# Kernel optimization log

Hardware: AMD Instinct MI355X
Metric: run time of the kernel (lower is better)

## Reference

```python
import jax, jax.numpy as jnp
import numpy as np

N_NODES = 200000
H_DIM = 64
OUT_DIM = 32
NUM_RELS = 8
NUM_BASES = 8
N_EDGES = 1000000


def setup_inputs() -> dict:
    key = jax.random.key(0)
    ks = jax.random.split(key, 10)
    emb = jax.random.normal(ks[0], (N_NODES, H_DIM), dtype=jnp.float32) * 0.1
    basis1 = jax.random.normal(ks[1], (NUM_BASES, H_DIM, H_DIM), dtype=jnp.float32) * 0.05
    comp1 = jax.random.normal(ks[2], (NUM_RELS, NUM_BASES), dtype=jnp.float32)
    bias1 = jnp.zeros((H_DIM,), dtype=jnp.float32)
    basis2 = jax.random.normal(ks[3], (NUM_BASES, H_DIM, OUT_DIM), dtype=jnp.float32) * 0.05
    comp2 = jax.random.normal(ks[4], (NUM_RELS, NUM_BASES), dtype=jnp.float32)
    bias2 = jnp.zeros((OUT_DIM,), dtype=jnp.float32)
    src = jax.random.randint(ks[5], (N_EDGES,), 0, N_NODES, dtype=jnp.int32)
    dst = jax.random.randint(ks[6], (N_EDGES,), 0, N_NODES, dtype=jnp.int32)
    etype = jax.random.randint(ks[7], (N_EDGES,), 0, NUM_RELS, dtype=jnp.int32)
    norm = jax.random.uniform(ks[8], (N_EDGES, 1), dtype=jnp.float32)
    return {"emb": emb, "basis1": basis1, "comp1": comp1, "bias1": bias1,
            "basis2": basis2, "comp2": comp2, "bias2": bias2,
            "src": src, "dst": dst, "etype": etype, "norm": norm}


def _rel_graph_conv(x, basis, comp, bias, src, dst, etype, norm, num_nodes):
    # basis regularizer: W_r = sum_b comp[r,b] * basis[b]  -> [R, in, out]
    W = jnp.einsum('rb,bio->rio', comp, basis)
    # transform all nodes under every relation: [R, N, out]
    y = jnp.einsum('ni,rio->rno', x, W)
    # per-edge message: gather transformed src feature for the edge's relation
    msg = y[etype, src] * norm  # [E, out]
    # scatter-sum to destination nodes
    agg = jax.ops.segment_sum(msg, dst, num_segments=num_nodes)
    return agg + bias


def reference(emb, basis1, comp1, bias1, basis2, comp2, bias2, src, dst, etype, norm):
    h = _rel_graph_conv(emb, basis1, comp1, bias1, src, dst, etype, norm, emb.shape[0])
    h = _rel_graph_conv(h, basis2, comp2, bias2, src, dst, etype, norm, emb.shape[0])
    return h
```

## Files before the change

kernel.cpp:

```cpp
#include <hip/hip_runtime.h>
#include <hip/hip_bf16.h>

#define NRELS 8
#define NB 8
#define PBLK 256
#define BSH 9
#define BCAP 3584

typedef __attribute__((ext_vector_type(8))) short short8v;
typedef __attribute__((ext_vector_type(4))) float f32x4;

__device__ __forceinline__ short bfc(float f) {
    __hip_bfloat16 h = __float2bfloat16(f);
    return *reinterpret_cast<short*>(&h);
}
__device__ __forceinline__ float bf2f(ushort u) {
    return __uint_as_float((unsigned)u << 16);
}
__device__ __forceinline__ short8v cvt8(float4 a, float4 b) {
    short8v r;
    r[0] = bfc(a.x); r[1] = bfc(a.y); r[2] = bfc(a.z); r[3] = bfc(a.w);
    r[4] = bfc(b.x); r[5] = bfc(b.y); r[6] = bfc(b.z); r[7] = bfc(b.w);
    return r;
}

__global__ void wprep_kernel(const float* __restrict__ basis1, const float* __restrict__ comp1,
                             const float* __restrict__ basis2, const float* __restrict__ comp2,
                             short* __restrict__ Wf1, short* __restrict__ Wf2) {
    int idx = blockIdx.x * blockDim.x + threadIdx.x;
    const int n1 = 64 * 512;
    const int n2 = 32 * 512;
    if (idx < n1) {
        int f = idx >> 9, lane = (idx >> 3) & 63, j = idx & 7;
        int ks = f & 1, q = (f >> 1) & 7, gg = f >> 4;
        int c = gg * 128 + 8 * (lane & 15) + q;
        int k = ks * 32 + (lane >> 4) * 8 + j;
        int r = c >> 6, crel = c & 63;
        float s = 0.f;
#pragma unroll
        for (int b = 0; b < NB; ++b)
            s = fmaf(comp1[r * NB + b], basis1[b * 4096 + k * 64 + crel], s);
        Wf1[idx] = bfc(s);
    } else if (idx < n1 + n2) {
        int i2 = idx - n1;
        int f = i2 >> 9, lane = (i2 >> 3) & 63, j = i2 & 7;
        int ks = f & 1, q = (f >> 1) & 7, gg = f >> 4;
        int c = gg * 128 + 8 * (lane & 15) + q;
        int k = ks * 32 + (lane >> 4) * 8 + j;
        int r = c >> 5, crel = c & 31;
        float s = 0.f;
#pragma unroll
        for (int b = 0; b < NB; ++b)
            s = fmaf(comp2[r * NB + b], basis2[b * 2048 + k * 32 + crel], s);
        Wf2[i2] = bfc(s);
    }
}

__global__ void histA_kernel(const int* __restrict__ dst, int* __restrict__ histM,
                             int nEdges, int nBuck, int chunk) {
    __shared__ int h[512];
    for (int t = threadIdx.x; t < nBuck; t += 256) h[t] = 0;
    __syncthreads();
    int start = blockIdx.x * chunk;
    int end = min(nEdges, start + chunk);
    for (int i = start + threadIdx.x; i < end; i += 256)
        atomicAdd(&h[dst[i] >> BSH], 1);
    __syncthreads();
    for (int t = threadIdx.x; t < nBuck; t += 256)
        histM[t * PBLK + blockIdx.x] = h[t];
}

__global__ void scanA_kernel(const int* __restrict__ histM, int* __restrict__ offs,
                             int* __restrict__ bucketBase, int nBuck, int nBlk, int nEdges) {
    __shared__ int tot[512];
    const int b = threadIdx.x;
    int s = 0;
    if (b < nBuck) {
        const int4* hp = (const int4*)(histM + b * nBlk);
        for (int k = 0; k < nBlk / 4; ++k) {
            int4 v = hp[k];
            s += v.x + v.y + v.z + v.w;
        }
    }
    tot[b] = s;
    __syncthreads();
    int own = s;
    for (int st = 1; st < 512; st <<= 1) {
        int t = (b >= st) ? tot[b - st] : 0;
        __syncthreads();
        tot[b] += t;
        __syncthreads();
    }
    int base = tot[b] - own;
    if (b < nBuck) {
        bucketBase[b] = base;
        int run = base;
        const int4* hp = (const int4*)(histM + b * nBlk);
        int4* op = (int4*)(offs + b * nBlk);
        for (int k = 0; k < nBlk / 4; ++k) {
            int4 h4 = hp[k];
            int4 o4;
            o4.x = run; run += h4.x;
            o4.y = run; run += h4.y;
            o4.z = run; run += h4.z;
            o4.w = run; run += h4.w;
            op[k] = o4;
        }
    }
    if (b == 0) bucketBase[nBuck] = nEdges;
}

__global__ void part_kernel(const int* __restrict__ src, const int* __restrict__ dst,
                            const int* __restrict__ et, const float* __restrict__ norm,
                            const int* __restrict__ offs, uint2* __restrict__ staged,
                            int nEdges, int nBuck, int chunk) {
    __shared__ int cur[512];
    for (int t = threadIdx.x; t < nBuck; t += 256)
        cur[t] = offs[t * PBLK + blockIdx.x];
    __syncthreads();
    int start = blockIdx.x * chunk;
    int end = min(nEdges, start + chunk);
    for (int i = start + threadIdx.x; i < end; i += 256) {
        int d = dst[i];
        int b = d >> BSH;
        int p = atomicAdd(&cur[b], 1);
        staged[p] = make_uint2(((unsigned)(d & 511) << 21) |
                               ((unsigned)src[i] << 3) | (unsigned)et[i],
                               __float_as_uint(norm[i]));
    }
}

__global__ void sortB_kernel(uint2* __restrict__ meta, const int* __restrict__ bucketBase,
                             int* __restrict__ endOff, int nNodes) {
    const int b = blockIdx.x;
    const int tid = threadIdx.x;
    const int e0 = bucketBase[b];
    const int n = min(bucketBase[b + 1] - e0, BCAP);
    __shared__ uint2 st[BCAP];
    __shared__ int h[512];
    __shared__ int pb[256];
    h[2 * tid] = 0; h[2 * tid + 1] = 0;
    __syncthreads();
    for (int j = tid; j < n; j += 256) {
        uint2 v = meta[e0 + j];
        st[j] = v;
        atomicAdd(&h[v.x >> 21], 1);
    }
    __syncthreads();
    int h0 = h[2 * tid], h1v = h[2 * tid + 1];
    int ps = h0 + h1v;
    pb[tid] = ps;
    __syncthreads();
    for (int s = 1; s < 256; s <<= 1) {
        int t = (tid >= s) ? pb[tid - s] : 0;
        __syncthreads();
        pb[tid] += t;
        __syncthreads();
    }
    int ex = pb[tid] - ps;
    int d0 = b << BSH;
    int dA = d0 + 2 * tid, dB = dA + 1;
    if (dA < nNodes) endOff[dA] = e0 + ex + h0;
    if (dB < nNodes) endOff[dB] = e0 + ex + ps;
    h[2 * tid] = ex;
    h[2 * tid + 1] = ex + h0;
    __syncthreads();
    for (int j = tid; j < n; j += 256) {
        uint2 v = st[j];
        int r = atomicAdd(&h[v.x >> 21], 1);
        meta[e0 + r] = make_uint2(v.x & 0x1FFFFFu, v.y);
    }
}

template <int G128, bool BF16IN>
__global__ __launch_bounds__(256) void transform_kernel(
    const void* __restrict__ xin, const short* __restrict__ Wf,
    ushort* __restrict__ yb, int nNodes) {
    constexpr int TOUT = G128 * 128;
    const int lane = threadIdx.x & 63;
    const int wid = (blockIdx.x * blockDim.x + threadIdx.x) >> 6;
    const int base = wid * 32;
    if (base >= nNodes) return;
    const int ml = lane & 15, kg = lane >> 4;

    short8v A[2][2];
#pragma unroll
    for (int s = 0; s < 2; ++s) {
        int row = min(base + s * 16 + ml, nNodes - 1);
        if (BF16IN) {
            const ushort* xp = (const ushort*)xin + (size_t)row * 64 + kg * 8;
            A[s][0] = *(const short8v*)xp;
            A[s][1] = *(const short8v*)(xp + 32);
        } else {
            const float* xp = (const float*)xin + (size_t)row * 64 + kg * 8;
            float4 f0 = *(const float4*)xp;
            float4 f1 = *(const float4*)(xp + 4);
            float4 f2 = *(const float4*)(xp + 32);
            float4 f3 = *(const float4*)(xp + 36);
            A[s][0] = cvt8(f0, f1);
            A[s][1] = cvt8(f2, f3);
        }
    }
#pragma unroll
    for (int gg = 0; gg < G128; ++gg) {
        const short* wp = Wf + (size_t)gg * 16 * 512 + lane * 8;
        f32x4 acc[2][8];
#pragma unroll
        for (int q = 0; q < 8; ++q) {
            short8v B0 = *(const short8v*)(wp + (q * 2 + 0) * 512);
            short8v B1 = *(const short8v*)(wp + (q * 2 + 1) * 512);
#pragma unroll
            for (int s = 0; s < 2; ++s) {
                acc[s][q] = __builtin_amdgcn_mfma_f32_16x16x32_bf16(A[s][0], B0,
                                                                    (f32x4){0.f, 0.f, 0.f, 0.f}, 0, 0, 0);
                acc[s][q] = __builtin_amdgcn_mfma_f32_16x16x32_bf16(A[s][1], B1, acc[s][q], 0, 0, 0);
            }
        }
#pragma unroll
        for (int s = 0; s < 2; ++s) {
#pragma unroll
            for (int i = 0; i < 4; ++i) {
                int row = base + s * 16 + kg * 4 + i;
                if (row < nNodes) {
                    uint4 pk;
                    pk.x = (unsigned)(ushort)bfc(acc[s][0][i]) | ((unsigned)(ushort)bfc(acc[s][1][i]) << 16);
                    pk.y = (unsigned)(ushort)bfc(acc[s][2][i]) | ((unsigned)(ushort)bfc(acc[s][3][i]) << 16);
                    pk.z = (unsigned)(ushort)bfc(acc[s][4][i]) | ((unsigned)(ushort)bfc(acc[s][5][i]) << 16);
                    pk.w = (unsigned)(ushort)bfc(acc[s][6][i]) | ((unsigned)(ushort)bfc(acc[s][7][i]) << 16);
                    *reinterpret_cast<uint4*>(yb + (size_t)row * TOUT + gg * 128 + ml * 8) = pk;
                }
            }
        }
    }
}

template <int OUT, typename OutT, bool ACCUM, bool FILTER, int SHIFT>
__global__ __launch_bounds__(256, 4) void edge_kernel(
    const ushort* __restrict__ yb, const uint2* __restrict__ meta,
    const int* __restrict__ endOff, const float* __restrict__ bias,
    OutT* __restrict__ out, int nNodes, int D, int rtLo) {
    const int lane = threadIdx.x & 63;

    if constexpr (!FILTER) {
        const int wid = (blockIdx.x * blockDim.x + threadIdx.x) >> 6;
        const int o = lane & (OUT - 1);
        const int d0 = wid * D;
        if (d0 >= nNodes) return;
        const int d1 = min(d0 + D, nNodes);
        const float bv = bias[o];

        int bndv = 0x7fffffff;
        if (lane < D) bndv = endOff[min(d0 + lane, nNodes - 1)];
        const int eEnd = __builtin_amdgcn_readlane(bndv, d1 - 1 - d0);
        int e = __builtin_amdgcn_readfirstlane((d0 == 0) ? 0 : endOff[d0 - 1]);
        int dcur = d0;
        int bnd = __builtin_amdgcn_readlane(bndv, 0);
        float acc = 0.f;

        auto gv = [&](unsigned key) -> float {
            const ushort* rowp = (const ushort*)((const char*)yb +
                                                 ((size_t)key << SHIFT));
            return bf2f(rowp[o]);
        };
        auto flushd = [&]() {
            size_t idx = (size_t)dcur * OUT + o;
            if (OUT == 64 || lane < OUT) {
                if constexpr (ACCUM)
                    out[idx] = (OutT)(ushort)bfc(bf2f((ushort)out[idx]) + acc);
                else if constexpr (sizeof(OutT) == 2)
                    out[idx] = (OutT)(ushort)bfc(bv + acc);
                else
                    out[idx] = (OutT)(bv + acc);
            }
            acc = 0.f;
            ++dcur;
            bnd = __builtin_amdgcn_readlane(bndv, dcur - d0);
        };

        if (e < eEnd) {
            const int eL = eEnd - 1;
            uint2 Ma[8], Mb[8];
            float Va[8];
#pragma unroll
            for (int k = 0; k < 8; ++k) Ma[k] = meta[min(e + k, eL)];
#pragma unroll
            for (int k = 0; k < 8; ++k) Mb[k] = meta[min(e + 8 + k, eL)];
#pragma unroll
            for (int k = 0; k < 8; ++k) Va[k] = gv(Ma[k].x);

            const int nFull = (eEnd - e) >> 3;
            for (int blk = 0; blk < nFull; ++blk) {
                float Vb[8];
                uint2 Mc[8];
#pragma unroll
                for (int k = 0; k < 8; ++k) Vb[k] = gv(Mb[k].x);
#pragma unroll
                for (int k = 0; k < 8; ++k) Mc[k] = meta[min(e + 16 + k, eL)];
#pragma unroll
                for (int k = 0; k < 8; ++k) {
                    while (e >= bnd) flushd();
                    acc = fmaf(__uint_as_float(Ma[k].y), Va[k], acc);
                    ++e;
                }
#pragma unroll
                for (int k = 0; k < 8; ++k) { Ma[k] = Mb[k]; Mb[k] = Mc[k]; Va[k] = Vb[k]; }
            }
            const int rem = eEnd - e;
#pragma unroll
            for (int k = 0; k < 8; ++k) {
                if (k < rem) {
                    while (e >= bnd) flushd();
                    acc = fmaf(__uint_as_float(Ma[k].y), Va[k], acc);
                    ++e;
                }
            }
        }
        while (dcur < d1) flushd();
    } else {
        constexpr int GPW = 64 / OUT;
        const int wid = (blockIdx.x * blockDim.x + threadIdx.x) >> 6;
        const int sub = (GPW == 2) ? (lane >> 5) : 0;
        const int gbase = sub << 5;
        const int gid = wid * GPW + sub;
        const int o = lane & (OUT - 1);
        const int d0 = gid * D;
        if (d0 >= nNodes) return;
        const int d1 = min(d0 + D, nNodes);
        const float bv = bias[o];

        int bndv = 0x7fffffff;
        if (o < D) bndv = endOff[min(d0 + o, nNodes - 1)];
        const int eEnd = __shfl(bndv, gbase + (d1 - 1 - d0));
        int e = (d0 == 0) ? 0 : endOff[d0 - 1];
        int dcur = d0;
        int bnd = __shfl(bndv, gbase);
        float acc = 0.f;

        auto gv = [&](unsigned key) -> float {
            int rr = (int)(key & 7u) - rtLo;
            if ((unsigned)rr >= 4u) return 0.f;
            unsigned off = (((key >> 3) * (unsigned)(4 * OUT)) +
                            (unsigned)rr * OUT + (unsigned)o) << 1;
            return bf2f(*(const ushort*)((const char*)yb + off));
        };
        auto flush = [&](int d, float a) {
            size_t idx = (size_t)d * OUT + o;
            if constexpr (ACCUM) {
                out[idx] = (OutT)(ushort)bfc(bf2f((ushort)out[idx]) + a);
            } else if constexpr (sizeof(OutT) == 2) {
                out[idx] = (OutT)(ushort)bfc(bv + a);
            } else {
                out[idx] = (OutT)(bv + a);
            }
        };

        if (e < eEnd) {
            const int eL = eEnd - 1;
            uint2 Ma[8], Mb[8];
            float Va[8];
#pragma unroll
            for (int k = 0; k < 8; ++k) Ma[k] = meta[min(e + k, eL)];
#pragma unroll
            for (int k = 0; k < 8; ++k) Mb[k] = meta[min(e + 8 + k, eL)];
#pragma unroll
            for (int k = 0; k < 8; ++k) Va[k] = gv(Ma[k].x);
            const int nFull = (eEnd - e) >> 3;
            for (int blk = 0; blk < nFull; ++blk) {
                float Vb[8];
                uint2 Mc[8];
#pragma unroll
                for (int k = 0; k < 8; ++k) Vb[k] = gv(Mb[k].x);
#pragma unroll
                for (int k = 0; k < 8; ++k) Mc[k] = meta[min(e + 16 + k, eL)];
#pragma unroll
                for (int k = 0; k < 8; ++k) {
                    while (e >= bnd) {
                        flush(dcur, acc); acc = 0.f; ++dcur;
                        bnd = __shfl(bndv, gbase + (dcur - d0));
                    }
                    acc = fmaf(__uint_as_float(Ma[k].y), Va[k], acc);
                    ++e;
                }
#pragma unroll
                for (int k = 0; k < 8; ++k) { Ma[k] = Mb[k]; Mb[k] = Mc[k]; Va[k] = Vb[k]; }
            }
            const int rem = eEnd - e;
#pragma unroll
            for (int k = 0; k < 8; ++k) {
                if (k < rem) {
                    while (e >= bnd) {
                        flush(dcur, acc); acc = 0.f; ++dcur;
                        bnd = __shfl(bndv, gbase + (dcur - d0));
                    }
                    acc = fmaf(__uint_as_float(Ma[k].y), Va[k], acc);
                    ++e;
                }
            }
        }
        for (; dcur < d1; ++dcur) {
            flush(dcur, acc);
            acc = 0.f;
        }
    }
}

extern "C" void kernel_launch(void* const* d_in, const int* in_sizes, int n_in,
                              void* d_out, int out_size, void* d_ws, size_t ws_size,
                              hipStream_t stream) {
    const float* emb    = (const float*)d_in[0];
    const float* basis1 = (const float*)d_in[1];
    const float* comp1  = (const float*)d_in[2];
    const float* bias1  = (const float*)d_in[3];
    const float* basis2 = (const float*)d_in[4];
    const float* comp2  = (const float*)d_in[5];
    const float* bias2  = (const float*)d_in[6];
    const int*   src    = (const int*)d_in[7];
    const int*   dst    = (const int*)d_in[8];
    const int*   etype  = (const int*)d_in[9];
    const float* norm   = (const float*)d_in[10];
    float* out = (float*)d_out;

    const int nNodes = in_sizes[0] / 64;
    const int nEdges = in_sizes[7];

    const int nBuck = (nNodes + 511) >> BSH;
    const int chunk = (nEdges + PBLK - 1) / PBLK;

    char* ws = (char*)d_ws;
    short* Wf1        = (short*)(ws);
    short* Wf2        = (short*)(ws + 65536);
    int*   histM      = (int*)(ws + 98304);
    int*   offs       = (int*)(ws + 498688);
    int*   bucketBase = (int*)(ws + 899072);
    int*   endOff     = (int*)(ws + 900640);
    size_t offMeta = 1703936;
    uint2* meta       = (uint2*)(ws + offMeta);
    size_t offY = offMeta + (size_t)nEdges * 8;

    const size_t yFused = (size_t)nNodes * 512 * 2;
    const size_t yHalf  = (size_t)nNodes * 256 * 2;
    const size_t h1Sz   = (size_t)nNodes * 64 * 2;
    const bool fused = ws_size >= offY + yFused + h1Sz;
    const size_t ySz = fused ? yFused : yHalf;
    ushort* yB  = (ushort*)(ws + offY);
    ushort* h1b = (ushort*)(ws + offY + ySz);

    wprep_kernel<<<192, 256, 0, stream>>>(basis1, comp1, basis2, comp2, Wf1, Wf2);
    histA_kernel<<<PBLK, 256, 0, stream>>>(dst, histM, nEdges, nBuck, chunk);
    scanA_kernel<<<1, 512, 0, stream>>>(histM, offs, bucketBase, nBuck, PBLK, nEdges);
    part_kernel<<<PBLK, 256, 0, stream>>>(src, dst, etype, norm, offs, meta,
                                          nEdges, nBuck, chunk);
    sortB_kernel<<<nBuck, 256, 0, stream>>>(meta, bucketBase, endOff, nNodes);

    const int tBlocks = (((nNodes + 31) / 32) + 3) / 4;
    const int D = 8;
    const int nGroups = (nNodes + D - 1) / D;
    const int gBlocks = (nGroups + 3) / 4;

    if (fused) {
        transform_kernel<4, false><<<tBlocks, 256, 0, stream>>>(emb, Wf1, yB, nNodes);
        edge_kernel<64, ushort, false, false, 7><<<gBlocks, 256, 0, stream>>>(
            yB, meta, endOff, bias1, h1b, nNodes, D, 0);
    } else {
        transform_kernel<2, false><<<tBlocks, 256, 0, stream>>>(emb, Wf1, yB, nNodes);
        edge_kernel<64, ushort, false, true, 0><<<gBlocks, 256, 0, stream>>>(
            yB, meta, endOff, bias1, h1b, nNodes, D, 0);
        transform_kernel<2, false><<<tBlocks, 256, 0, stream>>>(emb, Wf1 + 16384, yB, nNodes);
        edge_kernel<64, ushort, true, true, 0><<<gBlocks, 256, 0, stream>>>(
            yB, meta, endOff, bias1, h1b, nNodes, D, 4);
    }
    transform_kernel<2, true><<<tBlocks, 256, 0, stream>>>(h1b, Wf2, yB, nNodes);
    edge_kernel<32, float, false, false, 6><<<gBlocks, 256, 0, stream>>>(
        yB, meta, endOff, bias2, out, nNodes, D, 0);
}
```

Measured before the change: 244.1 us.

## Co-schedule layer-1 transform with sort preprocessing and split layer-2 pipeline

Splits the layer-1 node transform into four slices and fuses each slice into the histogram, scan, partition and bucket-sort launches as extra blocks. The small sort kernels then share the GPU with independent dense work instead of leaving CUs idle. It also splits layer-1 aggregation into node halves, so the layer-2 transform of the first half runs alongside the edge aggregation of the second half. This needs an extra y2 buffer and uses hand-tuned split ratios.

```diff
diff --git a/kernel.cpp b/kernel.cpp
--- a/kernel.cpp
+++ b/kernel.cpp
@@ -56,69 +56,81 @@
     }
 }
 
-__global__ void histA_kernel(const int* __restrict__ dst, int* __restrict__ histM,
-                             int nEdges, int nBuck, int chunk) {
+__device__ __forceinline__ void histA_body(const int* __restrict__ dst, int* __restrict__ histM,
+                                           int nEdges, int nBuck, int chunk, int bid) {
     __shared__ int h[512];
     for (int t = threadIdx.x; t < nBuck; t += 256) h[t] = 0;
     __syncthreads();
-    int start = blockIdx.x * chunk;
+    int start = bid * chunk;
     int end = min(nEdges, start + chunk);
     for (int i = start + threadIdx.x; i < end; i += 256)
         atomicAdd(&h[dst[i] >> BSH], 1);
     __syncthreads();
     for (int t = threadIdx.x; t < nBuck; t += 256)
-        histM[t * PBLK + blockIdx.x] = h[t];
-}
-
-__global__ void scanA_kernel(const int* __restrict__ histM, int* __restrict__ offs,
-                             int* __restrict__ bucketBase, int nBuck, int nBlk, int nEdges) {
+        histM[t * PBLK + bid] = h[t];
+}
+
+__device__ __forceinline__ void scanA_body(const int* __restrict__ histM, int* __restrict__ offs,
+                                           int* __restrict__ bucketBase, int nBuck, int nBlk,
+                                           int nEdges) {
     __shared__ int tot[512];
-    const int b = threadIdx.x;
-    int s = 0;
-    if (b < nBuck) {
-        const int4* hp = (const int4*)(histM + b * nBlk);
-        for (int k = 0; k < nBlk / 4; ++k) {
-            int4 v = hp[k];
-            s += v.x + v.y + v.z + v.w;
-        }
-    }
-    tot[b] = s;
-    __syncthreads();
-    int own = s;
+    const int tid = threadIdx.x;
+    int sums[2] = {0, 0};
+#pragma unroll
+    for (int half = 0; half < 2; ++half) {
+        int b = tid + half * 256;
+        if (b < nBuck) {
+            const int4* hp = (const int4*)(histM + b * nBlk);
+            int s = 0;
+            for (int k = 0; k < nBlk / 4; ++k) {
+                int4 v = hp[k];
+                s += v.x + v.y + v.z + v.w;
+            }
+            sums[half] = s;
+        }
+        tot[b] = sums[half];
+    }
+    __syncthreads();
     for (int st = 1; st < 512; st <<= 1) {
-        int t = (b >= st) ? tot[b - st] : 0;
+        int t0 = (tid >= st) ? tot[tid - st] : 0;
+        int t1 = tot[tid + 256 - st];
         __syncthreads();
-        tot[b] += t;
+        tot[tid] += t0;
+        tot[tid + 256] += t1;
         __syncthreads();
     }
-    int base = tot[b] - own;
-    if (b < nBuck) {
-        bucketBase[b] = base;
-        int run = base;
-        const int4* hp = (const int4*)(histM + b * nBlk);
-        int4* op = (int4*)(offs + b * nBlk);
-        for (int k = 0; k < nBlk / 4; ++k) {
-            int4 h4 = hp[k];
-            int4 o4;
-            o4.x = run; run += h4.x;
-            o4.y = run; run += h4.y;
-            o4.z = run; run += h4.z;
-            o4.w = run; run += h4.w;
-            op[k] = o4;
-        }
-    }
-    if (b == 0) bucketBase[nBuck] = nEdges;
-}
-
-__global__ void part_kernel(const int* __restrict__ src, const int* __restrict__ dst,
-                            const int* __restrict__ et, const float* __restrict__ norm,
-                            const int* __restrict__ offs, uint2* __restrict__ staged,
-                            int nEdges, int nBuck, int chunk) {
+#pragma unroll
+    for (int half = 0; half < 2; ++half) {
+        int b = tid + half * 256;
+        if (b < nBuck) {
+            int base = tot[b] - sums[half];
+            bucketBase[b] = base;
+            int run = base;
+            const int4* hp = (const int4*)(histM + b * nBlk);
+            int4* op = (int4*)(offs + b * nBlk);
+            for (int k = 0; k < nBlk / 4; ++k) {
+                int4 h4 = hp[k];
+                int4 o4;
+                o4.x = run; run += h4.x;
+                o4.y = run; run += h4.y;
+                o4.z = run; run += h4.z;
+                o4.w = run; run += h4.w;
+                op[k] = o4;
+            }
+        }
+    }
+    if (tid == 0) bucketBase[nBuck] = nEdges;
+}
+
+__device__ __forceinline__ void part_body(const int* __restrict__ src, const int* __restrict__ dst,
+                                          const int* __restrict__ et, const float* __restrict__ norm,
+                                          const int* __restrict__ offs, uint2* __restrict__ staged,
+                                          int nEdges, int nBuck, int chunk, int bid) {
     __shared__ int cur[512];
     for (int t = threadIdx.x; t < nBuck; t += 256)
-        cur[t] = offs[t * PBLK + blockIdx.x];
-    __syncthreads();
-    int start = blockIdx.x * chunk;
+        cur[t] = offs[t * PBLK + bid];
+    __syncthreads();
+    int start = bid * chunk;
     int end = min(nEdges, start + chunk);
     for (int i = start + threadIdx.x; i < end; i += 256) {
         int d = dst[i];
@@ -130,12 +142,12 @@
     }
 }
 
-__global__ void sortB_kernel(uint2* __restrict__ meta, const int* __restrict__ bucketBase,
-                             int* __restrict__ endOff, int nNodes) {
-    const int b = blockIdx.x;
+__device__ __forceinline__ void sortB_body(uint2* __restrict__ meta,
+                                           const int* __restrict__ bucketBase,
+                                           int* __restrict__ endOff, int nNodes, int bid) {
     const int tid = threadIdx.x;
-    const int e0 = bucketBase[b];
-    const int n = min(bucketBase[b + 1] - e0, BCAP);
+    const int e0 = bucketBase[bid];
+    const int n = min(bucketBase[bid + 1] - e0, BCAP);
     __shared__ uint2 st[BCAP];
     __shared__ int h[512];
     __shared__ int pb[256];
@@ -158,7 +170,7 @@
         __syncthreads();
     }
     int ex = pb[tid] - ps;
-    int d0 = b << BSH;
+    int d0 = bid << BSH;
     int dA = d0 + 2 * tid, dB = dA + 1;
     if (dA < nNodes) endOff[dA] = e0 + ex + h0;
     if (dB < nNodes) endOff[dB] = e0 + ex + ps;
@@ -173,12 +185,11 @@
 }
 
 template <int G128, bool BF16IN>
-__global__ __launch_bounds__(256) void transform_kernel(
-    const void* __restrict__ xin, const short* __restrict__ Wf,
-    ushort* __restrict__ yb, int nNodes) {
+__device__ __forceinline__ void transform_body(const void* __restrict__ xin,
+                                               const short* __restrict__ Wf,
+                                               ushort* __restrict__ yb, int nNodes, int wid) {
     constexpr int TOUT = G128 * 128;
     const int lane = threadIdx.x & 63;
-    const int wid = (blockIdx.x * blockDim.x + threadIdx.x) >> 6;
     const int base = wid * 32;
     if (base >= nNodes) return;
     const int ml = lane & 15, kg = lane >> 4;
@@ -234,174 +245,206 @@
     }
 }
 
-template <int OUT, typename OutT, bool ACCUM, bool FILTER, int SHIFT>
-__global__ __launch_bounds__(256, 4) void edge_kernel(
+template <int G128, bool BF16IN>
+__global__ __launch_bounds__(256) void transform_kernel(
+    const void* __restrict__ xin, const short* __restrict__ Wf,
+    ushort* __restrict__ yb, int nNodes, int waveOff) {
+    int wid = waveOff + blockIdx.x * 4 + (threadIdx.x >> 6);
+    transform_body<G128, BF16IN>(xin, Wf, yb, nNodes, wid);
+}
+
+template <int OUT, typename OutT, bool ACCUM, int SHIFT>
+__device__ __forceinline__ void edge_body(const ushort* __restrict__ yb,
+                                          const uint2* __restrict__ meta,
+                                          const int* __restrict__ endOff,
+                                          const float* __restrict__ bias,
+                                          OutT* __restrict__ out, int nNodes, int D,
+                                          int wid, int dLo, int dHi) {
+    const int lane = threadIdx.x & 63;
+    const int o = lane & (OUT - 1);
+    const int d0 = dLo + wid * D;
+    if (d0 >= dHi) return;
+    const int d1 = min(d0 + D, dHi);
+    const float bv = bias[o];
+
+    int bndv = 0x7fffffff;
+    if (lane < D) bndv = endOff[min(d0 + lane, nNodes - 1)];
+    const int eEnd = __builtin_amdgcn_readlane(bndv, d1 - 1 - d0);
+    int e = __builtin_amdgcn_readfirstlane((d0 == 0) ? 0 : endOff[d0 - 1]);
+    int dcur = d0;
+    int bnd = __builtin_amdgcn_readlane(bndv, 0);
+    float acc = 0.f;
+
+    auto gv = [&](unsigned key) -> float {
+        const ushort* rowp = (const ushort*)((const char*)yb + ((size_t)key << SHIFT));
+        return bf2f(rowp[o]);
+    };
+    auto flushd = [&]() {
+        size_t idx = (size_t)dcur * OUT + o;
+        if (OUT == 64 || lane < OUT) {
+            if constexpr (ACCUM)
+                out[idx] = (OutT)(ushort)bfc(bf2f((ushort)out[idx]) + acc);
+            else if constexpr (sizeof(OutT) == 2)
+                out[idx] = (OutT)(ushort)bfc(bv + acc);
+            else
+                out[idx] = (OutT)(bv + acc);
+        }
+        acc = 0.f;
+        ++dcur;
+        bnd = __builtin_amdgcn_readlane(bndv, dcur - d0);
+    };
+
+    if (e < eEnd) {
+        const int eL = eEnd - 1;
+        uint2 Ma[8], Mb[8];
+        float Va[8];
+#pragma unroll
+        for (int k = 0; k < 8; ++k) Ma[k] = meta[min(e + k, eL)];
+#pragma unroll
+        for (int k = 0; k < 8; ++k) Mb[k] = meta[min(e + 8 + k, eL)];
+#pragma unroll
+        for (int k = 0; k < 8; ++k) Va[k] = gv(Ma[k].x);
+
+        const int nFull = (eEnd - e) >> 3;
+        for (int blk = 0; blk < nFull; ++blk) {
+            float Vb[8];
+            uint2 Mc[8];
+#pragma unroll
+            for (int k = 0; k < 8; ++k) Vb[k] = gv(Mb[k].x);
+#pragma unroll
+            for (int k = 0; k < 8; ++k) Mc[k] = meta[min(e + 16 + k, eL)];
+#pragma unroll
+            for (int k = 0; k < 8; ++k) {
+                while (e >= bnd) flushd();
+                acc = fmaf(__uint_as_float(Ma[k].y), Va[k], acc);
+                ++e;
+            }
+#pragma unroll
+            for (int k = 0; k < 8; ++k) { Ma[k] = Mb[k]; Mb[k] = Mc[k]; Va[k] = Vb[k]; }
+        }
+        const int rem = eEnd - e;
+#pragma unroll
+        for (int k = 0; k < 8; ++k) {
+            if (k < rem) {
+                while (e >= bnd) flushd();
+                acc = fmaf(__uint_as_float(Ma[k].y), Va[k], acc);
+                ++e;
+            }
+        }
+    }
+    while (dcur < d1) flushd();
+}
+
+template <int OUT, typename OutT, int SHIFT>
+__global__ __launch_bounds__(256, 4) void edge_s_kernel(
+    const ushort* __restrict__ yb, const uint2* __restrict__ meta,
+    const int* __restrict__ endOff, const float* __restrict__ bias,
+    OutT* __restrict__ out, int nNodes, int dLo, int dHi) {
+    int wid = blockIdx.x * 4 + (threadIdx.x >> 6);
+    edge_body<OUT, OutT, false, SHIFT>(yb, meta, endOff, bias, out, nNodes, 8, wid, dLo, dHi);
+}
+
+template <int OUT, typename OutT, bool ACCUM>
+__global__ __launch_bounds__(256, 4) void edge_f_kernel(
     const ushort* __restrict__ yb, const uint2* __restrict__ meta,
     const int* __restrict__ endOff, const float* __restrict__ bias,
     OutT* __restrict__ out, int nNodes, int D, int rtLo) {
     const int lane = threadIdx.x & 63;
-
-    if constexpr (!FILTER) {
-        const int wid = (blockIdx.x * blockDim.x + threadIdx.x) >> 6;
-        const int o = lane & (OUT - 1);
-        const int d0 = wid * D;
-        if (d0 >= nNodes) return;
-        const int d1 = min(d0 + D, nNodes);
-        const float bv = bias[o];
-
-        int bndv = 0x7fffffff;
-        if (lane < D) bndv = endOff[min(d0 + lane, nNodes - 1)];
-        const int eEnd = __builtin_amdgcn_readlane(bndv, d1 - 1 - d0);
-        int e = __builtin_amdgcn_readfirstlane((d0 == 0) ? 0 : endOff[d0 - 1]);
-        int dcur = d0;
-        int bnd = __builtin_amdgcn_readlane(bndv, 0);
-        float acc = 0.f;
-
-        auto gv = [&](unsigned key) -> float {
-            const ushort* rowp = (const ushort*)((const char*)yb +
-                                                 ((size_t)key << SHIFT));
-            return bf2f(rowp[o]);
-        };
-        auto flushd = [&]() {
-            size_t idx = (size_t)dcur * OUT + o;
-            if (OUT == 64 || lane < OUT) {
-                if constexpr (ACCUM)
-                    out[idx] = (OutT)(ushort)bfc(bf2f((ushort)out[idx]) + acc);
-                else if constexpr (sizeof(OutT) == 2)
-                    out[idx] = (OutT)(ushort)bfc(bv + acc);
-                else
-                    out[idx] = (OutT)(bv + acc);
-            }
-            acc = 0.f;
-            ++dcur;
-            bnd = __builtin_amdgcn_readlane(bndv, dcur - d0);
-        };
-
-        if (e < eEnd) {
-            const int eL = eEnd - 1;
-            uint2 Ma[8], Mb[8];
-            float Va[8];
-#pragma unroll
-            for (int k = 0; k < 8; ++k) Ma[k] = meta[min(e + k, eL)];
-#pragma unroll
-            for (int k = 0; k < 8; ++k) Mb[k] = meta[min(e + 8 + k, eL)];
-#pragma unroll
-            for (int k = 0; k < 8; ++k) Va[k] = gv(Ma[k].x);
-
-            const int nFull = (eEnd - e) >> 3;
-            for (int blk = 0; blk < nFull; ++blk) {
-                float Vb[8];
-                uint2 Mc[8];
-#pragma unroll
-                for (int k = 0; k < 8; ++k) Vb[k] = gv(Mb[k].x);
-#pragma unroll
-                for (int k = 0; k < 8; ++k) Mc[k] = meta[min(e + 16 + k, eL)];
-#pragma unroll
-                for (int k = 0; k < 8; ++k) {
-                    while (e >= bnd) flushd();
-                    acc = fmaf(__uint_as_float(Ma[k].y), Va[k], acc);
-                    ++e;
-                }
-#pragma unroll
-                for (int k = 0; k < 8; ++k) { Ma[k] = Mb[k]; Mb[k] = Mc[k]; Va[k] = Vb[k]; }
-            }
-            const int rem = eEnd - e;
-#pragma unroll
-            for (int k = 0; k < 8; ++k) {
-                if (k < rem) {
-                    while (e >= bnd) flushd();
-                    acc = fmaf(__uint_as_float(Ma[k].y), Va[k], acc);
-                    ++e;
-                }
-            }
-        }
-        while (dcur < d1) flushd();
-    } else {
-        constexpr int GPW = 64 / OUT;
-        const int wid = (blockIdx.x * blockDim.x + threadIdx.x) >> 6;
-        const int sub = (GPW == 2) ? (lane >> 5) : 0;
-        const int gbase = sub << 5;
-        const int gid = wid * GPW + sub;
-        const int o = lane & (OUT - 1);
-        const int d0 = gid * D;
-        if (d0 >= nNodes) return;
-        const int d1 = min(d0 + D, nNodes);
-        const float bv = bias[o];
-
-        int bndv = 0x7fffffff;
-        if (o < D) bndv = endOff[min(d0 + o, nNodes - 1)];
-        const int eEnd = __shfl(bndv, gbase + (d1 - 1 - d0));
-        int e = (d0 == 0) ? 0 : endOff[d0 - 1];
-        int dcur = d0;
-        int bnd = __shfl(bndv, gbase);
-        float acc = 0.f;
-
-        auto gv = [&](unsigned key) -> float {
-            int rr = (int)(key & 7u) - rtLo;
-            if ((unsigned)rr >= 4u) return 0.f;
-            unsigned off = (((key >> 3) * (unsigned)(4 * OUT)) +
-                            (unsigned)rr * OUT + (unsigned)o) << 1;
-            return bf2f(*(const ushort*)((const char*)yb + off));
-        };
-        auto flush = [&](int d, float a) {
-            size_t idx = (size_t)d * OUT + o;
-            if constexpr (ACCUM) {
-                out[idx] = (OutT)(ushort)bfc(bf2f((ushort)out[idx]) + a);
-            } else if constexpr (sizeof(OutT) == 2) {
-                out[idx] = (OutT)(ushort)bfc(bv + a);
-            } else {
-                out[idx] = (OutT)(bv + a);
-            }
-        };
-
-        if (e < eEnd) {
-            const int eL = eEnd - 1;
-            uint2 Ma[8], Mb[8];
-            float Va[8];
-#pragma unroll
-            for (int k = 0; k < 8; ++k) Ma[k] = meta[min(e + k, eL)];
-#pragma unroll
-            for (int k = 0; k < 8; ++k) Mb[k] = meta[min(e + 8 + k, eL)];
-#pragma unroll
-            for (int k = 0; k < 8; ++k) Va[k] = gv(Ma[k].x);
-            const int nFull = (eEnd - e) >> 3;
-            for (int blk = 0; blk < nFull; ++blk) {
-                float Vb[8];
-                uint2 Mc[8];
-#pragma unroll
-                for (int k = 0; k < 8; ++k) Vb[k] = gv(Mb[k].x);
-#pragma unroll
-                for (int k = 0; k < 8; ++k) Mc[k] = meta[min(e + 16 + k, eL)];
-#pragma unroll
-                for (int k = 0; k < 8; ++k) {
-                    while (e >= bnd) {
-                        flush(dcur, acc); acc = 0.f; ++dcur;
-                        bnd = __shfl(bndv, gbase + (dcur - d0));
-                    }
-                    acc = fmaf(__uint_as_float(Ma[k].y), Va[k], acc);
-                    ++e;
-                }
-#pragma unroll
-                for (int k = 0; k < 8; ++k) { Ma[k] = Mb[k]; Mb[k] = Mc[k]; Va[k] = Vb[k]; }
-            }
-            const int rem = eEnd - e;
-#pragma unroll
-            for (int k = 0; k < 8; ++k) {
-                if (k < rem) {
-                    while (e >= bnd) {
-                        flush(dcur, acc); acc = 0.f; ++dcur;
-                        bnd = __shfl(bndv, gbase + (dcur - d0));
-                    }
-                    acc = fmaf(__uint_as_float(Ma[k].y), Va[k], acc);
-                    ++e;
-                }
-            }
-        }
-        for (; dcur < d1; ++dcur) {
-            flush(dcur, acc);
-            acc = 0.f;
-        }
-    }
+    constexpr int GPW = 64 / OUT;
+    const int wid = (blockIdx.x * blockDim.x + threadIdx.x) >> 6;
+    const int sub = (GPW == 2) ? (lane >> 5) : 0;
+    const int gbase = sub << 5;
+    const int gid = wid * GPW + sub;
+    const int o = lane & (OUT - 1);
+    const int d0 = gid * D;
+    if (d0 >= nNodes) return;
+    const int d1 = min(d0 + D, nNodes);
+    const float bv = bias[o];
+
+    int bndv = 0x7fffffff;
+    if (o < D) bndv = endOff[min(d0 + o, nNodes - 1)];
+    const int eEnd = __shfl(bndv, gbase + (d1 - 1 - d0));
+    int e = (d0 == 0) ? 0 : endOff[d0 - 1];
+    int dcur = d0;
+    int bnd = __shfl(bndv, gbase);
+    float acc = 0.f;
+
+    auto gv = [&](unsigned key) -> float {
+        int rr = (int)(key & 7u) - rtLo;
+        if ((unsigned)rr >= 4u) return 0.f;
+        unsigned off = (((key >> 3) * (unsigned)(4 * OUT)) + (unsigned)rr * OUT +
+                        (unsigned)o) << 1;
+        return bf2f(*(const ushort*)((const char*)yb + off));
+    };
+    auto flush = [&](int d, float a) {
+        size_t idx = (size_t)d * OUT + o;
+        if constexpr (ACCUM) out[idx] = (OutT)(ushort)bfc(bf2f((ushort)out[idx]) + a);
+        else if constexpr (sizeof(OutT) == 2) out[idx] = (OutT)(ushort)bfc(bv + a);
+        else out[idx] = (OutT)(bv + a);
+    };
+
+    for (; e < eEnd; ++e) {
+        uint2 M = meta[e];
+        while (e >= bnd) {
+            flush(dcur, acc); acc = 0.f; ++dcur;
+            bnd = __shfl(bndv, gbase + (dcur - d0));
+        }
+        acc = fmaf(__uint_as_float(M.y), gv(M.x), acc);
+    }
+    for (; dcur < d1; ++dcur) { flush(dcur, acc); acc = 0.f; }
+}
+
+__global__ __launch_bounds__(256) void mk1_kernel(const int* dst, int* histM, int nEdges,
+                                                  int nBuck, int chunk, const float* emb,
+                                                  const short* Wf1, ushort* yB, int nNodes,
+                                                  int waveOff) {
+    if ((int)blockIdx.x < PBLK) { histA_body(dst, histM, nEdges, nBuck, chunk, blockIdx.x); return; }
+    int wid = waveOff + ((int)blockIdx.x - PBLK) * 4 + ((int)threadIdx.x >> 6);
+    transform_body<4, false>(emb, Wf1, yB, nNodes, wid);
+}
+
+__global__ __launch_bounds__(256) void mk2_kernel(const int* histM, int* offs, int* bucketBase,
+                                                  int nBuck, int nEdges, const float* emb,
+                                                  const short* Wf1, ushort* yB, int nNodes,
+                                                  int waveOff) {
+    if (blockIdx.x == 0) { scanA_body(histM, offs, bucketBase, nBuck, PBLK, nEdges); return; }
+    int wid = waveOff + ((int)blockIdx.x - 1) * 4 + ((int)threadIdx.x >> 6);
+    transform_body<4, false>(emb, Wf1, yB, nNodes, wid);
+}
+
+__global__ __launch_bounds__(256) void mk3_kernel(const int* src, const int* dst, const int* et,
+                                                  const float* norm, const int* offs, uint2* meta,
+                                                  int nEdges, int nBuck, int chunk,
+                                                  const float* emb, const short* Wf1, ushort* yB,
+                                                  int nNodes, int waveOff) {
+    if ((int)blockIdx.x < PBLK) {
+        part_body(src, dst, et, norm, offs, meta, nEdges, nBuck, chunk, blockIdx.x);
+        return;
+    }
+    int wid = waveOff + ((int)blockIdx.x - PBLK) * 4 + ((int)threadIdx.x >> 6);
+    transform_body<4, false>(emb, Wf1, yB, nNodes, wid);
+}
+
+__global__ __launch_bounds__(256) void mk4_kernel(uint2* meta, const int* bucketBase, int* endOff,
+                                                  int nNodes, int nBuck, const float* emb,
+                                                  const short* Wf1, ushort* yB, int waveOff) {
+    if ((int)blockIdx.x < nBuck) { sortB_body(meta, bucketBase, endOff, nNodes, blockIdx.x); return; }
+    int wid = waveOff + ((int)blockIdx.x - nBuck) * 4 + ((int)threadIdx.x >> 6);
+    transform_body<4, false>(emb, Wf1, yB, nNodes, wid);
+}
+
+__global__ __launch_bounds__(256, 4) void mk6_kernel(const ushort* yB, const uint2* meta,
+                                                     const int* endOff, const float* bias1,
+                                                     ushort* h1b, const short* Wf2, ushort* y2,
+                                                     int nNodes, int eBlocks, int dLo, int dHi,
+                                                     int capNodes) {
+    if ((int)blockIdx.x < eBlocks) {
+        int wid = blockIdx.x * 4 + (threadIdx.x >> 6);
+        edge_body<64, ushort, false, 7>(yB, meta, endOff, bias1, h1b, nNodes, 8, wid, dLo, dHi);
+        return;
+    }
+    int wid = ((int)blockIdx.x - eBlocks) * 4 + ((int)threadIdx.x >> 6);
+    transform_body<2, true>(h1b, Wf2, y2, capNodes, wid);
 }
 
 extern "C" void kernel_launch(void* const* d_in, const int* in_sizes, int n_in,
@@ -439,37 +482,71 @@
 
     const size_t yFused = (size_t)nNodes * 512 * 2;
     const size_t yHalf  = (size_t)nNodes * 256 * 2;
+    const size_t y2Sz   = (size_t)nNodes * 256 * 2;
     const size_t h1Sz   = (size_t)nNodes * 64 * 2;
     const bool fused = ws_size >= offY + yFused + h1Sz;
-    const size_t ySz = fused ? yFused : yHalf;
-    ushort* yB  = (ushort*)(ws + offY);
-    ushort* h1b = (ushort*)(ws + offY + ySz);
+    const bool pipe  = ws_size >= offY + yFused + y2Sz + h1Sz;
+    ushort* yB = (ushort*)(ws + offY);
+    ushort* y2 = pipe ? (ushort*)(ws + offY + yFused) : yB;
+    ushort* h1b = pipe ? (ushort*)(ws + offY + yFused + y2Sz)
+                       : (ushort*)(ws + offY + (fused ? yFused : yHalf));
 
     wprep_kernel<<<192, 256, 0, stream>>>(basis1, comp1, basis2, comp2, Wf1, Wf2);
-    histA_kernel<<<PBLK, 256, 0, stream>>>(dst, histM, nEdges, nBuck, chunk);
-    scanA_kernel<<<1, 512, 0, stream>>>(histM, offs, bucketBase, nBuck, PBLK, nEdges);
-    part_kernel<<<PBLK, 256, 0, stream>>>(src, dst, etype, norm, offs, meta,
-                                          nEdges, nBuck, chunk);
-    sortB_kernel<<<nBuck, 256, 0, stream>>>(meta, bucketBase, endOff, nNodes);
-
-    const int tBlocks = (((nNodes + 31) / 32) + 3) / 4;
+
+    const int WT = (nNodes + 31) / 32;
+    const int wA = WT * 13 / 100, bA = (wA + 3) / 4;
+    const int wB = WT * 10 / 100, bB = (wB + 3) / 4;
+    const int wC = WT * 37 / 100, bC = (wC + 3) / 4;
+    const int offB = bA * 4, offC = offB + bB * 4, offD = offC + bC * 4;
+    const int remD = WT > offD ? WT - offD : 0;
+    const int bD = (remD + 3) / 4;
+    const int tA = fused ? bA : 0, tB = fused ? bB : 0, tC = fused ? bC : 0, tD = fused ? bD : 0;
+
+    mk1_kernel<<<PBLK + tA, 256, 0, stream>>>(dst, histM, nEdges, nBuck, chunk,
+                                              emb, Wf1, yB, nNodes, 0);
+    mk2_kernel<<<1 + tB, 256, 0, stream>>>(histM, offs, bucketBase, nBuck, nEdges,
+                                           emb, Wf1, yB, nNodes, offB);
+    mk3_kernel<<<PBLK + tC, 256, 0, stream>>>(src, dst, etype, norm, offs, meta,
+                                              nEdges, nBuck, chunk, emb, Wf1, yB, nNodes, offC);
+    mk4_kernel<<<nBuck + tD, 256, 0, stream>>>(meta, bucketBase, endOff, nNodes, nBuck,
+                                               emb, Wf1, yB, offD);
+
     const int D = 8;
-    const int nGroups = (nNodes + D - 1) / D;
-    const int gBlocks = (nGroups + 3) / 4;
-
-    if (fused) {
-        transform_kernel<4, false><<<tBlocks, 256, 0, stream>>>(emb, Wf1, yB, nNodes);
-        edge_kernel<64, ushort, false, false, 7><<<gBlocks, 256, 0, stream>>>(
+    if (fused && pipe) {
+        const int nHalf = ((nNodes / 2) + 31) / 32 * 32;
+        const int ebLo = ((nHalf / D) + 3) / 4;
+        const int gHi = (nNodes - nHalf + D - 1) / D;
+        const int ebHi = (gHi + 3) / 4;
+        const int wLo = nHalf / 32;
+        const int tbLo = (wLo + 3) / 4;
+        const int tbHi = ((WT - wLo) + 3) / 4;
+        edge_s_kernel<64, ushort, 7><<<ebLo, 256, 0, stream>>>(
+            yB, meta, endOff, bias1, h1b, nNodes, 0, nHalf);
+        mk6_kernel<<<ebHi + tbLo, 256, 0, stream>>>(
+            yB, meta, endOff, bias1, h1b, Wf2, y2, nNodes, ebHi, nHalf, nNodes, nHalf);
+        transform_kernel<2, true><<<tbHi, 256, 0, stream>>>(h1b, Wf2, y2, nNodes, wLo);
+        const int b32 = ((nNodes + D - 1) / D + 3) / 4;
+        edge_s_kernel<32, float, 6><<<b32, 256, 0, stream>>>(
+            y2, meta, endOff, bias2, out, nNodes, 0, nNodes);
+    } else if (fused) {
+        const int b64 = ((nNodes + D - 1) / D + 3) / 4;
+        edge_s_kernel<64, ushort, 7><<<b64, 256, 0, stream>>>(
+            yB, meta, endOff, bias1, h1b, nNodes, 0, nNodes);
+        const int tb = (WT + 3) / 4;
+        transform_kernel<2, true><<<tb, 256, 0, stream>>>(h1b, Wf2, yB, nNodes, 0);
+        edge_s_kernel<32, float, 6><<<b64, 256, 0, stream>>>(
+            yB, meta, endOff, bias2, out, nNodes, 0, nNodes);
+    } else {
+        const int tb = (WT + 3) / 4;
+        const int gBlocks = ((nNodes + D - 1) / D + 3) / 4;
+        transform_kernel<2, false><<<tb, 256, 0, stream>>>(emb, Wf1, yB, nNodes, 0);
+        edge_f_kernel<64, ushort, false><<<gBlocks, 256, 0, stream>>>(
             yB, meta, endOff, bias1, h1b, nNodes, D, 0);
-    } else {
-        transform_kernel<2, false><<<tBlocks, 256, 0, stream>>>(emb, Wf1, yB, nNodes);
-        edge_kernel<64, ushort, false, true, 0><<<gBlocks, 256, 0, stream>>>(
-            yB, meta, endOff, bias1, h1b, nNodes, D, 0);
-        transform_kernel<2, false><<<tBlocks, 256, 0, stream>>>(emb, Wf1 + 16384, yB, nNodes);
-        edge_kernel<64, ushort, true, true, 0><<<gBlocks, 256, 0, stream>>>(
+        transform_kernel<2, false><<<tb, 256, 0, stream>>>(emb, Wf1 + 16384, yB, nNodes, 0);
+        edge_f_kernel<64, ushort, true><<<gBlocks, 256, 0, stream>>>(
             yB, meta, endOff, bias1, h1b, nNodes, D, 4);
-    }
-    transform_kernel<2, true><<<tBlocks, 256, 0, stream>>>(h1b, Wf2, yB, nNodes);
-    edge_kernel<32, float, false, false, 6><<<gBlocks, 256, 0, stream>>>(
-        yB, meta, endOff, bias2, out, nNodes, D, 0);
-}
+        transform_kernel<2, true><<<tb, 256, 0, stream>>>(h1b, Wf2, yB, nNodes, 0);
+        edge_s_kernel<32, float, 6><<<gBlocks, 256, 0, stream>>>(
+            yB, meta, endOff, bias2, out, nNodes, 0, nNodes);
+    }
+}
```

Measured after the change: 244.5 us. About the same (+0.2%).
